# Kernel tuning notes

Hardware: AMD Instinct MI355X
Metric: run time of the kernel (lower is better)

The kernel has to match this reference:

```python
import jax, jax.numpy as jnp
import numpy as np

N, E, D, H, EF = 50000, 800000, 64, 64, 16


def setup_inputs() -> dict:
    key = jax.random.key(0)
    ks = jax.random.split(key, 12)
    s = 0.05
    return {
        "node_feat": jax.random.normal(ks[0], (N, D), jnp.float32),
        "coord": jax.random.normal(ks[1], (N, 3), jnp.float32),
        "edge_feat": jax.random.normal(ks[2], (E, EF), jnp.float32),
        "src": jax.random.randint(ks[3], (E,), 0, N, jnp.int32),
        "dst": jax.random.randint(ks[4], (E,), 0, N, jnp.int32),
        "W_e1": jax.random.normal(ks[5], (2 * D + EF + 1, H), jnp.float32) * s,
        "b_e1": jnp.zeros((H,), jnp.float32),
        "W_e2": jax.random.normal(ks[6], (H, H), jnp.float32) * s,
        "b_e2": jnp.zeros((H,), jnp.float32),
        "W_n1": jax.random.normal(ks[7], (D + H, H), jnp.float32) * s,
        "b_n1": jnp.zeros((H,), jnp.float32),
        "W_n2": jax.random.normal(ks[8], (H, D), jnp.float32) * s,
        "b_n2": jnp.zeros((D,), jnp.float32),
    }


def reference(node_feat, coord, edge_feat, src, dst,
              W_e1, b_e1, W_e2, b_e2, W_n1, b_n1, W_n2, b_n2):
    # per-edge radial distance: ||coord_src - coord_dst||^2  -> [E,1]
    x_diff = coord[src] - coord[dst]
    radial = jnp.sum(x_diff * x_diff, axis=-1, keepdims=True)
    # edge message MLP: concat [h_src, h_dst, radial, a] -> SiLU MLP
    f = jnp.concatenate([node_feat[src], node_feat[dst], radial, edge_feat], axis=-1)
    m = jax.nn.silu(f @ W_e1 + b_e1)
    msg = jax.nn.silu(m @ W_e2 + b_e2)  # [E,H]
    # scatter-sum aggregation to destination nodes
    h_neigh = jax.ops.segment_sum(msg, dst, num_segments=node_feat.shape[0])
    # node update MLP
    z = jnp.concatenate([node_feat, h_neigh], axis=-1)
    h = jax.nn.silu(z @ W_n1 + b_n1) @ W_n2 + b_n2
    return h
```

## Files before the change

kernel.cpp:

```cpp
#include <hip/hip_runtime.h>

#define D 64
#define H 64
#define EFD 16
#define MS 68
#define TE 128
#define TN 128
#define DPB 16
#define REFW 20

__device__ __forceinline__ float silu(float x) {
    return x / (1.0f + __expf(-x));
}

#define GEMM_STEP(acc_, a_, bf_) do { \
    const float* bp_ = (const float*)(bf_); \
    acc_[0] += (a_).x*bp_[0] + (a_).y*bp_[4] + (a_).z*bp_[8]  + (a_).w*bp_[12]; \
    acc_[1] += (a_).x*bp_[1] + (a_).y*bp_[5] + (a_).z*bp_[9]  + (a_).w*bp_[13]; \
    acc_[2] += (a_).x*bp_[2] + (a_).y*bp_[6] + (a_).z*bp_[10] + (a_).w*bp_[14]; \
    acc_[3] += (a_).x*bp_[3] + (a_).y*bp_[7] + (a_).z*bp_[11] + (a_).w*bp_[15]; \
} while (0)

#define PGEMM64(acc_, Wp_, wrow0_, eg_, hg_, smem_) do { \
    for (int k4 = 0; k4 < 16; k4++) { \
        float4 bf_[4]; \
        _Pragma("unroll") \
        for (int kk = 0; kk < 4; kk++) \
            bf_[kk] = *(const float4*)&(Wp_)[(size_t)((wrow0_) + 4*k4 + kk) * H + 4*(hg_)]; \
        _Pragma("unroll") \
        for (int i = 0; i < 8; i++) { \
            float4 a_ = *(const float4*)&(smem_)[(8*(eg_) + i) * MS + 4*k4]; \
            GEMM_STEP(acc_[i], a_, bf_); \
        } \
    } \
} while (0)


__global__ __launch_bounds__(256) void hist_kernel(
    const int* __restrict__ dst, int* __restrict__ deg, int E)
{
    int e = blockIdx.x * 256 + threadIdx.x;
    if (e < E) atomicAdd(&deg[dst[e]], 1);
}


__global__ __launch_bounds__(256) void scanA_kernel(
    const int* __restrict__ deg, int* __restrict__ part, int N)
{
    __shared__ int tmp[256];
    const int tid = threadIdx.x;
    int idx = blockIdx.x * 256 + tid;
    tmp[tid] = (idx < N) ? deg[idx] : 0;
    __syncthreads();
    for (int off = 128; off > 0; off >>= 1) {
        if (tid < off) tmp[tid] += tmp[tid + off];
        __syncthreads();
    }
    if (tid == 0) part[blockIdx.x] = tmp[0];
}

__global__ __launch_bounds__(256, 1) void scanB_kernel(
    int* __restrict__ part, int nparts)
{
    __shared__ int tmp[256];
    __shared__ int carry_s;
    const int tid = threadIdx.x;
    if (tid == 0) carry_s = 0;
    __syncthreads();
    for (int base = 0; base < nparts; base += 256) {
        int idx = base + tid;
        int v = (idx < nparts) ? part[idx] : 0;
        tmp[tid] = v;
        __syncthreads();
        #pragma unroll
        for (int off = 1; off < 256; off <<= 1) {
            int t = (tid >= off) ? tmp[tid - off] : 0;
            __syncthreads();
            tmp[tid] += t;
            __syncthreads();
        }
        int incl = tmp[tid];
        int tot = tmp[255];
        if (idx < nparts) part[idx] = carry_s + incl - v;
        __syncthreads();
        if (tid == 0) carry_s += tot;
        __syncthreads();
    }
}

__global__ __launch_bounds__(256) void scanC_kernel(
    const int* __restrict__ deg, const int* __restrict__ part,
    int* __restrict__ cursor, int N)
{
    __shared__ int tmp[256];
    const int tid = threadIdx.x;
    int idx = blockIdx.x * 256 + tid;
    int v = (idx < N) ? deg[idx] : 0;
    tmp[tid] = v;
    __syncthreads();
    #pragma unroll
    for (int off = 1; off < 256; off <<= 1) {
        int t = (tid >= off) ? tmp[tid - off] : 0;
        __syncthreads();
        tmp[tid] += t;
        __syncthreads();
    }
    if (idx < N) cursor[idx] = part[blockIdx.x] + tmp[tid] - v;
}


__global__ __launch_bounds__(256) void build3_kernel(
    const int* __restrict__ dst, const int* __restrict__ src,
    const float* __restrict__ coord, const float* __restrict__ edge_feat,
    int* __restrict__ cursor,
    int* __restrict__ srcs, int* __restrict__ dsts, float* __restrict__ refr,
    int E)
{
    int e = blockIdx.x * 256 + threadIdx.x;
    if (e >= E) return;
    int d2 = dst[e];
    int s = src[e];
    int pos = atomicAdd(&cursor[d2], 1);
    srcs[pos] = s;
    dsts[pos] = d2;
    float dx = coord[s*3+0] - coord[d2*3+0];
    float dy = coord[s*3+1] - coord[d2*3+1];
    float dz = coord[s*3+2] - coord[d2*3+2];
    float* rr = &refr[(size_t)pos * REFW];
    const float4* ef = (const float4*)&edge_feat[(size_t)e * EFD];
    *(float4*)&rr[0]  = ef[0];
    *(float4*)&rr[4]  = ef[1];
    *(float4*)&rr[8]  = ef[2];
    *(float4*)&rr[12] = ef[3];
    rr[16] = dx*dx + dy*dy + dz*dz;
}

__global__ __launch_bounds__(256) void build2_kernel(
    const int* __restrict__ dst, const int* __restrict__ src,
    int* __restrict__ cursor,
    int* __restrict__ eidx, int* __restrict__ srcs, int* __restrict__ dsts,
    int E)
{
    int e = blockIdx.x * 256 + threadIdx.x;
    if (e < E) {
        int d2 = dst[e];
        int pos = atomicAdd(&cursor[d2], 1);
        eidx[pos] = e;
        srcs[pos] = src[e];
        dsts[pos] = d2;
    }
}


__global__ __launch_bounds__(256, 4) void pre_kernel(
    const float* __restrict__ node_feat,
    const float* __restrict__ W_e1, const float* __restrict__ b_e1,
    float* __restrict__ Pa, float* __restrict__ Pb, int N)
{
    __shared__ float smem[TN * MS];
    const int tid = threadIdx.x;
    const int nbase = blockIdx.x * TN;
    const int ng = tid >> 4, hg = tid & 15, k = tid & 63, no = tid >> 6;

    #pragma unroll
    for (int t = 0; t < 32; t++) {
        int gn = nbase + no + 4*t;
        int cg = (gn < N) ? gn : (N - 1);
        smem[(no + 4*t) * MS + k] = node_feat[(size_t)cg * D + k];
    }
    __syncthreads();

    float accA[8][4], accB[8][4];
    {
        float4 b0 = *(const float4*)&b_e1[4*hg];
        #pragma unroll
        for (int i = 0; i < 8; i++) {
            accA[i][0]=b0.x; accA[i][1]=b0.y; accA[i][2]=b0.z; accA[i][3]=b0.w;
            accB[i][0]=0.f;  accB[i][1]=0.f;  accB[i][2]=0.f;  accB[i][3]=0.f;
        }
    }
    PGEMM64(accA, W_e1, 0,  ng, hg, smem);
    PGEMM64(accB, W_e1, 64, ng, hg, smem);

    #pragma unroll
    for (int i = 0; i < 8; i++) {
        int gn = nbase + 8*ng + i;
        if (gn < N) {
            float4 a; a.x=accA[i][0]; a.y=accA[i][1]; a.z=accA[i][2]; a.w=accA[i][3];
            float4 b; b.x=accB[i][0]; b.y=accB[i][1]; b.z=accB[i][2]; b.w=accB[i][3];
            *(float4*)&Pa[(size_t)gn * H + 4*hg] = a;
            *(float4*)&Pb[(size_t)gn * H + 4*hg] = b;
        }
    }
}


__global__ __launch_bounds__(256, 3) void edge_kernel3(
    const float* __restrict__ Pa, const float* __restrict__ Pb,
    const int* __restrict__ srcs, const int* __restrict__ dsts,
    const float* __restrict__ refr,
    const int* __restrict__ cursor_end, const int* __restrict__ deg,
    const float* __restrict__ W_e1,
    const float* __restrict__ W_e2, const float* __restrict__ b_e2,
    float* __restrict__ h_neigh, int N)
{
    __shared__ float smem[TE * MS];
    __shared__ float hacc[DPB * H];

    const int tid = threadIdx.x;
    const int dst0 = blockIdx.x * DPB;
    const int dlast = min(dst0 + DPB, N) - 1;
    const int rs = cursor_end[dst0] - deg[dst0];
    const int re = cursor_end[dlast];

    for (int i = tid; i < DPB * H; i += 256) hacc[i] = 0.f;

    const int eg = tid >> 4, hg = tid & 15;

    float acc[8][4];
    int dl[8];

    #define LOAD_TILE(base_, acc_, dl_) do { \
        _Pragma("unroll") \
        for (int i_ = 0; i_ < 8; i_++) { \
            int p_ = (base_) + 8*eg + i_; \
            bool val_ = (p_ < re); \
            int pp_ = val_ ? p_ : (re - 1); \
            int s_ = srcs[pp_]; \
            int d2_ = dsts[pp_]; \
            float4 pa_ = *(const float4*)&Pa[(size_t)s_ * H + 4*hg]; \
            float4 pb_ = *(const float4*)&Pb[(size_t)d2_ * H + 4*hg]; \
            acc_[i_][0] = pa_.x + pb_.x; acc_[i_][1] = pa_.y + pb_.y; \
            acc_[i_][2] = pa_.z + pb_.z; acc_[i_][3] = pa_.w + pb_.w; \
            dl_[i_] = val_ ? (d2_ - dst0) : -1; \
        } \
    } while (0)

    if (re > rs) LOAD_TILE(rs, acc, dl);

    for (int base = rs; base < re; base += TE) {
        for (int k4 = 0; k4 < 4; k4++) {
            float4 bf[4];
            #pragma unroll
            for (int kk = 0; kk < 4; kk++)
                bf[kk] = *(const float4*)&W_e1[(size_t)(129 + 4*k4 + kk) * H + 4*hg];
            #pragma unroll
            for (int i = 0; i < 8; i++) {
                int p = base + 8*eg + i;
                int pp = (p < re) ? p : (re - 1);
                float4 a = *(const float4*)&refr[(size_t)pp * REFW + 4*k4];
                GEMM_STEP(acc[i], a, bf);
            }
        }
        {
            float4 b = *(const float4*)&W_e1[(size_t)128 * H + 4*hg];
            #pragma unroll
            for (int i = 0; i < 8; i++) {
                int p = base + 8*eg + i;
                int pp = (p < re) ? p : (re - 1);
                float a = refr[(size_t)pp * REFW + 16];
                acc[i][0] += a*b.x; acc[i][1] += a*b.y;
                acc[i][2] += a*b.z; acc[i][3] += a*b.w;
            }
        }

        #pragma unroll
        for (int i = 0; i < 8; i++) {
            float4 mv;
            mv.x = silu(acc[i][0]); mv.y = silu(acc[i][1]);
            mv.z = silu(acc[i][2]); mv.w = silu(acc[i][3]);
            *(float4*)&smem[(8*eg+i)*MS + 4*hg] = mv;
        }

        float nacc[8][4]; int ndl[8];
        const int nb = base + TE;
        if (nb < re) LOAD_TILE(nb, nacc, ndl);

        __syncthreads();

        float acc2[8][4];
        {
            float4 b0 = *(const float4*)&b_e2[4*hg];
            #pragma unroll
            for (int i = 0; i < 8; i++) {
                acc2[i][0]=b0.x; acc2[i][1]=b0.y; acc2[i][2]=b0.z; acc2[i][3]=b0.w;
            }
        }
        PGEMM64(acc2, W_e2, 0, eg, hg, smem);

        float rx=0.f, ry=0.f, rz=0.f, rw=0.f;
        int cur = -1;
        #pragma unroll
        for (int i = 0; i < 8; i++) {
            int d = dl[i];
            if (d < 0) continue;
            float vx = silu(acc2[i][0]), vy = silu(acc2[i][1]);
            float vz = silu(acc2[i][2]), vw = silu(acc2[i][3]);
            if (d != cur) {
                if (cur >= 0) {
                    float* hp = &hacc[cur * H + 4*hg];
                    atomicAdd(&hp[0], rx); atomicAdd(&hp[1], ry);
                    atomicAdd(&hp[2], rz); atomicAdd(&hp[3], rw);
                }
                cur = d; rx = vx; ry = vy; rz = vz; rw = vw;
            } else {
                rx += vx; ry += vy; rz += vz; rw += vw;
            }
        }
        if (cur >= 0) {
            float* hp = &hacc[cur * H + 4*hg];
            atomicAdd(&hp[0], rx); atomicAdd(&hp[1], ry);
            atomicAdd(&hp[2], rz); atomicAdd(&hp[3], rw);
        }

        __syncthreads();

        #pragma unroll
        for (int i = 0; i < 8; i++) {
            acc[i][0]=nacc[i][0]; acc[i][1]=nacc[i][1];
            acc[i][2]=nacc[i][2]; acc[i][3]=nacc[i][3];
            dl[i]=ndl[i];
        }
    }

    __syncthreads();
    {
        const int dloc = tid >> 4, ch = 4 * (tid & 15);
        int gd = dst0 + dloc;
        if (gd < N) {
            float4 v = *(const float4*)&hacc[dloc * H + ch];
            *(float4*)&h_neigh[(size_t)gd * H + ch] = v;
        }
    }
    #undef LOAD_TILE
}


__global__ __launch_bounds__(256, 4) void edge_kernel2(
    const float* __restrict__ Pa, const float* __restrict__ Pb,
    const float* __restrict__ coord,
    const float* __restrict__ edge_feat,
    const int* __restrict__ eidx, const int* __restrict__ srcs,
    const int* __restrict__ dsts,
    const int* __restrict__ cursor_end, const int* __restrict__ deg,
    const float* __restrict__ W_e1,
    const float* __restrict__ W_e2, const float* __restrict__ b_e2,
    float* __restrict__ h_neigh, int N)
{
    __shared__ float smem[TE * MS];
    __shared__ float hacc[DPB * H];
    __shared__ int ssrc[TE], sdlo[TE], seid[TE];

    const int tid = threadIdx.x;
    const int dst0 = blockIdx.x * DPB;
    const int dlast = min(dst0 + DPB, N) - 1;
    const int rs = cursor_end[dst0] - deg[dst0];
    const int re = cursor_end[dlast];

    for (int i = tid; i < DPB * H; i += 256) hacc[i] = 0.f;

    const int eg = tid >> 4, hg = tid & 15;

    for (int base = rs; base < re; base += TE) {
        const int cnt = min(re - base, TE);
        __syncthreads();

        if (tid < TE) {
            int e = 0, s = 0, dlv = -1;
            float radial = 0.f;
            if (tid < cnt) {
                int p = base + tid;
                e = eidx[p]; s = srcs[p];
                int d2 = dsts[p]; dlv = d2 - dst0;
                float dx = coord[s*3+0] - coord[d2*3+0];
                float dy = coord[s*3+1] - coord[d2*3+1];
                float dz = coord[s*3+2] - coord[d2*3+2];
                radial = dx*dx + dy*dy + dz*dz;
            }
            ssrc[tid] = s; sdlo[tid] = dlv; seid[tid] = e;
            smem[tid * MS + 0] = radial;
        }
        __syncthreads();

        {
            const int k2 = tid & 15, e2 = tid >> 4;
            #pragma unroll
            for (int t = 0; t < 8; t++) {
                int r = e2 + 16*t;
                float v = (sdlo[r] >= 0) ? edge_feat[(size_t)seid[r] * EFD + k2] : 0.f;
                smem[r * MS + 1 + k2] = v;
            }
        }

        float acc[8][4];
        #pragma unroll
        for (int i = 0; i < 8; i++) {
            int r = 8*eg + i;
            int s = ssrc[r];
            int dlv = sdlo[r];
            int drow = (dlv >= 0) ? (dst0 + dlv) : 0;
            float4 pa = *(const float4*)&Pa[(size_t)s * H + 4*hg];
            float4 pb = *(const float4*)&Pb[(size_t)drow * H + 4*hg];
            acc[i][0] = pa.x + pb.x; acc[i][1] = pa.y + pb.y;
            acc[i][2] = pa.z + pb.z; acc[i][3] = pa.w + pb.w;
        }
        __syncthreads();

        for (int k4 = 0; k4 < 4; k4++) {
            float4 bf[4];
            #pragma unroll
            for (int kk = 0; kk < 4; kk++)
                bf[kk] = *(const float4*)&W_e1[(size_t)(128 + 4*k4 + kk) * H + 4*hg];
            #pragma unroll
            for (int i = 0; i < 8; i++) {
                float4 a = *(const float4*)&smem[(8*eg + i) * MS + 4*k4];
                GEMM_STEP(acc[i], a, bf);
            }
        }
        {
            float4 b = *(const float4*)&W_e1[(size_t)144 * H + 4*hg];
            #pragma unroll
            for (int i = 0; i < 8; i++) {
                float a = smem[(8*eg+i)*MS + 16];
                acc[i][0] += a*b.x; acc[i][1] += a*b.y; acc[i][2] += a*b.z; acc[i][3] += a*b.w;
            }
        }
        __syncthreads();

        #pragma unroll
        for (int i = 0; i < 8; i++) {
            float4 mv;
            mv.x = silu(acc[i][0]); mv.y = silu(acc[i][1]);
            mv.z = silu(acc[i][2]); mv.w = silu(acc[i][3]);
            *(float4*)&smem[(8*eg+i)*MS + 4*hg] = mv;
        }
        __syncthreads();

        float acc2[8][4];
        {
            float4 b0 = *(const float4*)&b_e2[4*hg];
            #pragma unroll
            for (int i = 0; i < 8; i++) {
                acc2[i][0]=b0.x; acc2[i][1]=b0.y; acc2[i][2]=b0.z; acc2[i][3]=b0.w;
            }
        }
        PGEMM64(acc2, W_e2, 0, eg, hg, smem);

        float rx=0.f, ry=0.f, rz=0.f, rw=0.f;
        int cur = -1;
        #pragma unroll
        for (int i = 0; i < 8; i++) {
            int r = 8*eg + i;
            int dlv = sdlo[r];
            if (dlv < 0) continue;
            float vx = silu(acc2[i][0]), vy = silu(acc2[i][1]);
            float vz = silu(acc2[i][2]), vw = silu(acc2[i][3]);
            if (dlv != cur) {
                if (cur >= 0) {
                    float* hp = &hacc[cur * H + 4*hg];
                    atomicAdd(&hp[0], rx); atomicAdd(&hp[1], ry);
                    atomicAdd(&hp[2], rz); atomicAdd(&hp[3], rw);
                }
                cur = dlv; rx = vx; ry = vy; rz = vz; rw = vw;
            } else {
                rx += vx; ry += vy; rz += vz; rw += vw;
            }
        }
        if (cur >= 0) {
            float* hp = &hacc[cur * H + 4*hg];
            atomicAdd(&hp[0], rx); atomicAdd(&hp[1], ry);
            atomicAdd(&hp[2], rz); atomicAdd(&hp[3], rw);
        }
    }

    __syncthreads();
    {
        const int dloc = tid >> 4, ch = 4 * (tid & 15);
        int gd = dst0 + dloc;
        if (gd < N) {
            float4 v = *(const float4*)&hacc[dloc * H + ch];
            *(float4*)&h_neigh[(size_t)gd * H + ch] = v;
        }
    }
}


__global__ __launch_bounds__(256, 4) void node_kernel(
    const float* __restrict__ node_feat,
    const float* __restrict__ h_neigh,
    const float* __restrict__ W_n1, const float* __restrict__ b_n1,
    const float* __restrict__ W_n2, const float* __restrict__ b_n2,
    float* __restrict__ out, int N)
{
    __shared__ float smem[TN * MS];

    const int tid = threadIdx.x;
    const int nbase = blockIdx.x * TN;

    const int ng = tid >> 4, hg = tid & 15, k = tid & 63, no = tid >> 6;

    float acc[8][4];
    {
        float4 b0 = *(const float4*)&b_n1[4*hg];
        #pragma unroll
        for (int i = 0; i < 8; i++) {
            acc[i][0]=b0.x; acc[i][1]=b0.y; acc[i][2]=b0.z; acc[i][3]=b0.w;
        }
    }

    float rA[32];
    #pragma unroll
    for (int t = 0; t < 32; t++) {
        int gn = nbase + no + 4*t;
        int cg = (gn < N) ? gn : (N - 1);
        rA[t] = node_feat[(size_t)cg * D + k];
    }
    #pragma unroll
    for (int t = 0; t < 32; t++)
        smem[(no + 4*t) * MS + k] = rA[t];
    __syncthreads();

    float rB[32];
    #pragma unroll
    for (int t = 0; t < 32; t++) {
        int gn = nbase + no + 4*t;
        int cg = (gn < N) ? gn : (N - 1);
        rB[t] = h_neigh[(size_t)cg * H + k];
    }
    PGEMM64(acc, W_n1, 0, ng, hg, smem);
    __syncthreads();

    #pragma unroll
    for (int t = 0; t < 32; t++)
        smem[(no + 4*t) * MS + k] = rB[t];
    __syncthreads();

    PGEMM64(acc, W_n1, 64, ng, hg, smem);
    __syncthreads();

    #pragma unroll
    for (int i = 0; i < 8; i++) {
        float4 mv;
        mv.x = silu(acc[i][0]); mv.y = silu(acc[i][1]);
        mv.z = silu(acc[i][2]); mv.w = silu(acc[i][3]);
        *(float4*)&smem[(8*ng+i)*MS + 4*hg] = mv;
    }
    __syncthreads();

    float acc2[8][4];
    {
        float4 b0 = *(const float4*)&b_n2[4*hg];
        #pragma unroll
        for (int i = 0; i < 8; i++) {
            acc2[i][0]=b0.x; acc2[i][1]=b0.y; acc2[i][2]=b0.z; acc2[i][3]=b0.w;
        }
    }
    PGEMM64(acc2, W_n2, 0, ng, hg, smem);

    #pragma unroll
    for (int i = 0; i < 8; i++) {
        int gn = nbase + 8*ng + i;
        if (gn < N) {
            float4 ov;
            ov.x = acc2[i][0]; ov.y = acc2[i][1]; ov.z = acc2[i][2]; ov.w = acc2[i][3];
            *(float4*)&out[(size_t)gn * D + 4*hg] = ov;
        }
    }
}

extern "C" void kernel_launch(void* const* d_in, const int* in_sizes, int n_in,
                              void* d_out, int out_size, void* d_ws, size_t ws_size,
                              hipStream_t stream)
{
    const float* node_feat = (const float*)d_in[0];
    const float* coord     = (const float*)d_in[1];
    const float* edge_feat = (const float*)d_in[2];
    const int*   src       = (const int*)d_in[3];
    const int*   dst       = (const int*)d_in[4];
    const float* W_e1 = (const float*)d_in[5];
    const float* b_e1 = (const float*)d_in[6];
    const float* W_e2 = (const float*)d_in[7];
    const float* b_e2 = (const float*)d_in[8];
    const float* W_n1 = (const float*)d_in[9];
    const float* b_n1 = (const float*)d_in[10];
    const float* W_n2 = (const float*)d_in[11];
    const float* b_n2 = (const float*)d_in[12];

    const int N = in_sizes[0] / D;
    const int E = in_sizes[3];
    const int NP = (N + 255) / 256;

    const size_t hn_b  = (size_t)N * H * sizeof(float);
    const size_t n_i   = (size_t)N * sizeof(int);
    const size_t e_i   = (size_t)E * sizeof(int);
    const size_t pt_b  = 1024 * sizeof(int);
    const size_t p_b   = (size_t)N * H * sizeof(float);
    const size_t rf_b  = (size_t)E * REFW * sizeof(float);

    const size_t need3 = hn_b + 2*n_i + pt_b + 2*e_i + rf_b + 2*p_b;
    const size_t need2 = hn_b + 2*n_i + pt_b + 3*e_i + 2*p_b;

    float* h_neigh = (float*)d_ws;
    const int dblocks = (N + DPB - 1) / DPB;

    if (ws_size >= need3) {
        char* p = (char*)d_ws + hn_b;
        int* deg    = (int*)p;   p += n_i;
        int* cursor = (int*)p;   p += n_i;
        int* part   = (int*)p;   p += pt_b;
        int* srcs   = (int*)p;   p += e_i;
        int* dsts   = (int*)p;   p += e_i;
        float* refr = (float*)p; p += rf_b;
        float* Pa   = (float*)p; p += p_b;
        float* Pb   = (float*)p;

        hipMemsetAsync(deg, 0, n_i, stream);
        hist_kernel<<<(E + 255) / 256, 256, 0, stream>>>(dst, deg, E);
        scanA_kernel<<<NP, 256, 0, stream>>>(deg, part, N);
        scanB_kernel<<<1, 256, 0, stream>>>(part, NP);
        scanC_kernel<<<NP, 256, 0, stream>>>(deg, part, cursor, N);
        build3_kernel<<<(E + 255) / 256, 256, 0, stream>>>(dst, src, coord, edge_feat,
                                                           cursor, srcs, dsts, refr, E);
        pre_kernel<<<(N + TN - 1) / TN, 256, 0, stream>>>(node_feat, W_e1, b_e1,
                                                          Pa, Pb, N);
        edge_kernel3<<<dblocks, 256, 0, stream>>>(Pa, Pb, srcs, dsts, refr,
                                                  cursor, deg,
                                                  W_e1, W_e2, b_e2, h_neigh, N);
    } else {
        char* p = (char*)d_ws + hn_b;
        int* deg    = (int*)p;   p += n_i;
        int* cursor = (int*)p;   p += n_i;
        int* part   = (int*)p;   p += pt_b;
        int* eidx   = (int*)p;   p += e_i;
        int* srcs   = (int*)p;   p += e_i;
        int* dsts   = (int*)p;   p += e_i;
        float* Pa   = (float*)p; p += p_b;
        float* Pb   = (float*)p;

        hipMemsetAsync(deg, 0, n_i, stream);
        hist_kernel<<<(E + 255) / 256, 256, 0, stream>>>(dst, deg, E);
        scanA_kernel<<<NP, 256, 0, stream>>>(deg, part, N);
        scanB_kernel<<<1, 256, 0, stream>>>(part, NP);
        scanC_kernel<<<NP, 256, 0, stream>>>(deg, part, cursor, N);
        build2_kernel<<<(E + 255) / 256, 256, 0, stream>>>(dst, src, cursor,
                                                           eidx, srcs, dsts, E);
        pre_kernel<<<(N + TN - 1) / TN, 256, 0, stream>>>(node_feat, W_e1, b_e1,
                                                          Pa, Pb, N);
        edge_kernel2<<<dblocks, 256, 0, stream>>>(Pa, Pb, coord, edge_feat,
                                                  eidx, srcs, dsts, cursor, deg,
                                                  W_e1, W_e2, b_e2, h_neigh, N);
    }

    const int nblocks = (N + TN - 1) / TN;
    node_kernel<<<nblocks, 256, 0, stream>>>(node_feat, h_neigh,
                                             W_n1, b_n1, W_n2, b_n2,
                                             (float*)d_out, N);
}
```

Before: 610.4 us.

## Run second edge MLP GEMM on bf16 MFMA with wave-local swizzled LDS tiles

```diff
diff --git a/kernel.cpp b/kernel.cpp
--- a/kernel.cpp
+++ b/kernel.cpp
@@ -7,10 +7,20 @@
 #define TE 128
 #define TN 128
 #define DPB 16
+#define DPB4 32
 #define REFW 20
+
+typedef __attribute__((ext_vector_type(8))) short bf16x8;
+typedef __attribute__((ext_vector_type(4))) float f32x4;
 
 __device__ __forceinline__ float silu(float x) {
     return x / (1.0f + __expf(-x));
+}
+
+__device__ __forceinline__ short f2bf(float x) {
+    union { float f; unsigned u; } c; c.f = x;
+    unsigned r = c.u + 0x7fffu + ((c.u >> 16) & 1u);
+    return (short)(r >> 16);
 }
 
 #define GEMM_STEP(acc_, a_, bf_) do { \
@@ -195,7 +205,7 @@
 }
 
 
-__global__ __launch_bounds__(256, 3) void edge_kernel3(
+__global__ __launch_bounds__(256, 3) void edge_kernel4(
     const float* __restrict__ Pa, const float* __restrict__ Pb,
     const int* __restrict__ srcs, const int* __restrict__ dsts,
     const float* __restrict__ refr,
@@ -204,41 +214,53 @@
     const float* __restrict__ W_e2, const float* __restrict__ b_e2,
     float* __restrict__ h_neigh, int N)
 {
-    __shared__ float smem[TE * MS];
-    __shared__ float hacc[DPB * H];
+    __shared__ alignas(16) short mt[TE * H];
+    __shared__ float hacc[DPB4 * H];
 
     const int tid = threadIdx.x;
-    const int dst0 = blockIdx.x * DPB;
-    const int dlast = min(dst0 + DPB, N) - 1;
+    const int lane = tid & 63;
+    const int wv = tid >> 6;
+    const int lg = lane >> 4;
+    const int lc = lane & 15;
+    const int eg = tid >> 4;
+    const int hg = tid & 15;
+
+    const int dst0 = blockIdx.x * DPB4;
+    const int dlast = min(dst0 + DPB4, N) - 1;
     const int rs = cursor_end[dst0] - deg[dst0];
     const int re = cursor_end[dlast];
 
-    for (int i = tid; i < DPB * H; i += 256) hacc[i] = 0.f;
-
-    const int eg = tid >> 4, hg = tid & 15;
-
-    float acc[8][4];
-    int dl[8];
-
-    #define LOAD_TILE(base_, acc_, dl_) do { \
-        _Pragma("unroll") \
-        for (int i_ = 0; i_ < 8; i_++) { \
-            int p_ = (base_) + 8*eg + i_; \
-            bool val_ = (p_ < re); \
-            int pp_ = val_ ? p_ : (re - 1); \
-            int s_ = srcs[pp_]; \
-            int d2_ = dsts[pp_]; \
-            float4 pa_ = *(const float4*)&Pa[(size_t)s_ * H + 4*hg]; \
-            float4 pb_ = *(const float4*)&Pb[(size_t)d2_ * H + 4*hg]; \
-            acc_[i_][0] = pa_.x + pb_.x; acc_[i_][1] = pa_.y + pb_.y; \
-            acc_[i_][2] = pa_.z + pb_.z; acc_[i_][3] = pa_.w + pb_.w; \
-            dl_[i_] = val_ ? (d2_ - dst0) : -1; \
-        } \
-    } while (0)
-
-    if (re > rs) LOAD_TILE(rs, acc, dl);
+    for (int i = tid; i < DPB4 * H; i += 256) hacc[i] = 0.f;
+
+    bf16x8 bfr[2][4];
+    #pragma unroll
+    for (int ks = 0; ks < 2; ks++)
+        #pragma unroll
+        for (int nf = 0; nf < 4; nf++) {
+            bf16x8 v;
+            #pragma unroll
+            for (int t = 0; t < 8; t++)
+                v[t] = f2bf(W_e2[(size_t)(lg*8 + t + 32*ks) * H + 16*nf + lc]);
+            bfr[ks][nf] = v;
+        }
+    float bias[4];
+    #pragma unroll
+    for (int nf = 0; nf < 4; nf++) bias[nf] = b_e2[16*nf + lc];
+
+    __syncthreads();
 
     for (int base = rs; base < re; base += TE) {
+        float a1[8][4];
+        #pragma unroll
+        for (int i = 0; i < 8; i++) {
+            int p = base + 8*eg + i;
+            int pp = (p < re) ? p : (re - 1);
+            int s = srcs[pp], d2 = dsts[pp];
+            float4 pa = *(const float4*)&Pa[(size_t)s * H + 4*hg];
+            float4 pb = *(const float4*)&Pb[(size_t)d2 * H + 4*hg];
+            a1[i][0] = pa.x + pb.x; a1[i][1] = pa.y + pb.y;
+            a1[i][2] = pa.z + pb.z; a1[i][3] = pa.w + pb.w;
+        }
         for (int k4 = 0; k4 < 4; k4++) {
             float4 bf[4];
             #pragma unroll
@@ -249,7 +271,7 @@
                 int p = base + 8*eg + i;
                 int pp = (p < re) ? p : (re - 1);
                 float4 a = *(const float4*)&refr[(size_t)pp * REFW + 4*k4];
-                GEMM_STEP(acc[i], a, bf);
+                GEMM_STEP(a1[i], a, bf);
             }
         }
         {
@@ -259,80 +281,93 @@
                 int p = base + 8*eg + i;
                 int pp = (p < re) ? p : (re - 1);
                 float a = refr[(size_t)pp * REFW + 16];
-                acc[i][0] += a*b.x; acc[i][1] += a*b.y;
-                acc[i][2] += a*b.z; acc[i][3] += a*b.w;
-            }
-        }
-
-        #pragma unroll
-        for (int i = 0; i < 8; i++) {
-            float4 mv;
-            mv.x = silu(acc[i][0]); mv.y = silu(acc[i][1]);
-            mv.z = silu(acc[i][2]); mv.w = silu(acc[i][3]);
-            *(float4*)&smem[(8*eg+i)*MS + 4*hg] = mv;
-        }
-
-        float nacc[8][4]; int ndl[8];
-        const int nb = base + TE;
-        if (nb < re) LOAD_TILE(nb, nacc, ndl);
-
-        __syncthreads();
-
-        float acc2[8][4];
-        {
-            float4 b0 = *(const float4*)&b_e2[4*hg];
-            #pragma unroll
-            for (int i = 0; i < 8; i++) {
-                acc2[i][0]=b0.x; acc2[i][1]=b0.y; acc2[i][2]=b0.z; acc2[i][3]=b0.w;
-            }
-        }
-        PGEMM64(acc2, W_e2, 0, eg, hg, smem);
-
-        float rx=0.f, ry=0.f, rz=0.f, rw=0.f;
-        int cur = -1;
-        #pragma unroll
-        for (int i = 0; i < 8; i++) {
-            int d = dl[i];
-            if (d < 0) continue;
-            float vx = silu(acc2[i][0]), vy = silu(acc2[i][1]);
-            float vz = silu(acc2[i][2]), vw = silu(acc2[i][3]);
-            if (d != cur) {
-                if (cur >= 0) {
-                    float* hp = &hacc[cur * H + 4*hg];
-                    atomicAdd(&hp[0], rx); atomicAdd(&hp[1], ry);
-                    atomicAdd(&hp[2], rz); atomicAdd(&hp[3], rw);
+                a1[i][0] += a*b.x; a1[i][1] += a*b.y;
+                a1[i][2] += a*b.z; a1[i][3] += a*b.w;
+            }
+        }
+
+        #pragma unroll
+        for (int i = 0; i < 8; i++) {
+            short4 mv;
+            mv.x = f2bf(silu(a1[i][0])); mv.y = f2bf(silu(a1[i][1]));
+            mv.z = f2bf(silu(a1[i][2])); mv.w = f2bf(silu(a1[i][3]));
+            int row = 8*eg + i;
+            int sidx = (row * H + 4*hg) ^ (i << 3);
+            *(short4*)&mt[sidx] = mv;
+        }
+        asm volatile("s_waitcnt lgkmcnt(0)" ::: "memory");
+
+        bf16x8 afr[2][2];
+        #pragma unroll
+        for (int mf = 0; mf < 2; mf++)
+            #pragma unroll
+            for (int ks = 0; ks < 2; ks++) {
+                int row = 32*wv + 16*mf + lc;
+                int sidx = (row * H + lg*8 + 32*ks) ^ ((lc & 7) << 3);
+                afr[mf][ks] = *(const bf16x8*)&mt[sidx];
+            }
+        f32x4 c2[2][4];
+        #pragma unroll
+        for (int mf = 0; mf < 2; mf++)
+            #pragma unroll
+            for (int nf = 0; nf < 4; nf++) {
+                f32x4 cinit = {bias[nf], bias[nf], bias[nf], bias[nf]};
+                c2[mf][nf] = cinit;
+            }
+        #pragma unroll
+        for (int ks = 0; ks < 2; ks++)
+            #pragma unroll
+            for (int mf = 0; mf < 2; mf++)
+                #pragma unroll
+                for (int nf = 0; nf < 4; nf++)
+                    c2[mf][nf] = __builtin_amdgcn_mfma_f32_16x16x32_bf16(
+                        afr[mf][ks], bfr[ks][nf], c2[mf][nf], 0, 0, 0);
+
+        #pragma unroll
+        for (int mf = 0; mf < 2; mf++) {
+            int rb = 32*wv + 16*mf + 4*lg;
+            int cur = -1;
+            float s0 = 0.f, s1 = 0.f, s2 = 0.f, s3 = 0.f;
+            #pragma unroll
+            for (int reg = 0; reg < 4; reg++) {
+                int p = base + rb + reg;
+                if (p < re) {
+                    int dl = dsts[p] - dst0;
+                    float v0 = silu(c2[mf][0][reg]);
+                    float v1 = silu(c2[mf][1][reg]);
+                    float v2 = silu(c2[mf][2][reg]);
+                    float v3 = silu(c2[mf][3][reg]);
+                    if (dl != cur) {
+                        if (cur >= 0) {
+                            atomicAdd(&hacc[cur*H + lc],      s0);
+                            atomicAdd(&hacc[cur*H + 16 + lc], s1);
+                            atomicAdd(&hacc[cur*H + 32 + lc], s2);
+                            atomicAdd(&hacc[cur*H + 48 + lc], s3);
+                        }
+                        cur = dl; s0 = v0; s1 = v1; s2 = v2; s3 = v3;
+                    } else { s0 += v0; s1 += v1; s2 += v2; s3 += v3; }
                 }
-                cur = d; rx = vx; ry = vy; rz = vz; rw = vw;
-            } else {
-                rx += vx; ry += vy; rz += vz; rw += vw;
-            }
-        }
-        if (cur >= 0) {
-            float* hp = &hacc[cur * H + 4*hg];
-            atomicAdd(&hp[0], rx); atomicAdd(&hp[1], ry);
-            atomicAdd(&hp[2], rz); atomicAdd(&hp[3], rw);
-        }
-
-        __syncthreads();
-
-        #pragma unroll
-        for (int i = 0; i < 8; i++) {
-            acc[i][0]=nacc[i][0]; acc[i][1]=nacc[i][1];
-            acc[i][2]=nacc[i][2]; acc[i][3]=nacc[i][3];
-            dl[i]=ndl[i];
-        }
-    }
-
-    __syncthreads();
-    {
-        const int dloc = tid >> 4, ch = 4 * (tid & 15);
+            }
+            if (cur >= 0) {
+                atomicAdd(&hacc[cur*H + lc],      s0);
+                atomicAdd(&hacc[cur*H + 16 + lc], s1);
+                atomicAdd(&hacc[cur*H + 32 + lc], s2);
+                atomicAdd(&hacc[cur*H + 48 + lc], s3);
+            }
+        }
+    }
+
+    __syncthreads();
+    #pragma unroll
+    for (int t = 0; t < 2; t++) {
+        int idx = tid + t*256;
+        int dloc = idx >> 4;
+        int ch = (idx & 15) * 4;
         int gd = dst0 + dloc;
-        if (gd < N) {
-            float4 v = *(const float4*)&hacc[dloc * H + ch];
-            *(float4*)&h_neigh[(size_t)gd * H + ch] = v;
-        }
-    }
-    #undef LOAD_TILE
+        if (gd < N)
+            *(float4*)&h_neigh[(size_t)gd * H + ch] =
+                *(const float4*)&hacc[dloc * H + ch];
+    }
 }
 
 
@@ -598,10 +633,8 @@
     const size_t rf_b  = (size_t)E * REFW * sizeof(float);
 
     const size_t need3 = hn_b + 2*n_i + pt_b + 2*e_i + rf_b + 2*p_b;
-    const size_t need2 = hn_b + 2*n_i + pt_b + 3*e_i + 2*p_b;
 
     float* h_neigh = (float*)d_ws;
-    const int dblocks = (N + DPB - 1) / DPB;
 
     if (ws_size >= need3) {
         char* p = (char*)d_ws + hn_b;
@@ -623,7 +656,8 @@
                                                            cursor, srcs, dsts, refr, E);
         pre_kernel<<<(N + TN - 1) / TN, 256, 0, stream>>>(node_feat, W_e1, b_e1,
                                                           Pa, Pb, N);
-        edge_kernel3<<<dblocks, 256, 0, stream>>>(Pa, Pb, srcs, dsts, refr,
+        const int dblocks = (N + DPB4 - 1) / DPB4;
+        edge_kernel4<<<dblocks, 256, 0, stream>>>(Pa, Pb, srcs, dsts, refr,
                                                   cursor, deg,
                                                   W_e1, W_e2, b_e2, h_neigh, N);
     } else {
@@ -646,9 +680,10 @@
                                                            eidx, srcs, dsts, E);
         pre_kernel<<<(N + TN - 1) / TN, 256, 0, stream>>>(node_feat, W_e1, b_e1,
                                                           Pa, Pb, N);
-        edge_kernel2<<<dblocks, 256, 0, stream>>>(Pa, Pb, coord, edge_feat,
-                                                  eidx, srcs, dsts, cursor, deg,
-                                                  W_e1, W_e2, b_e2, h_neigh, N);
+        const int dblocks2 = (N + DPB - 1) / DPB;
+        edge_kernel2<<<dblocks2, 256, 0, stream>>>(Pa, Pb, coord, edge_feat,
+                                                   eidx, srcs, dsts, cursor, deg,
+                                                   W_e1, W_e2, b_e2, h_neigh, N);
     }
 
     const int nblocks = (N + TN - 1) / TN;
```

Result: faster. 525.8 us (-13.9%).
